# Optimization experiments

Hardware: AMD Instinct MI355X
Metric: run time of the kernel (lower is better)

Reference implementation:

```python
import jax, jax.numpy as jnp
import numpy as np

EMBED_DIM = 256
NUM_HEADS = 8
HEAD_DIM = EMBED_DIM // NUM_HEADS
ADJ_CHANNELS = 4
B, N = 8, 1024


def setup_inputs() -> dict:
    key = jax.random.key(0)
    ks = jax.random.split(key, 12)
    s = 1.0 / np.sqrt(EMBED_DIM)
    sa = 1.0 / np.sqrt(ADJ_CHANNELS)
    return {
        "x": jax.random.normal(ks[0], (B, N, EMBED_DIM), dtype=jnp.float32),
        "adj": jax.random.uniform(ks[1], (B, N, N, ADJ_CHANNELS), dtype=jnp.float32),
        "Wq": jax.random.uniform(ks[2], (EMBED_DIM, EMBED_DIM), jnp.float32, -s, s),
        "bq": jnp.zeros((EMBED_DIM,), jnp.float32),
        "Wk": jax.random.uniform(ks[3], (EMBED_DIM, EMBED_DIM), jnp.float32, -s, s),
        "bk": jnp.zeros((EMBED_DIM,), jnp.float32),
        "Wv": jax.random.uniform(ks[4], (EMBED_DIM, EMBED_DIM), jnp.float32, -s, s),
        "bv": jnp.zeros((EMBED_DIM,), jnp.float32),
        "Wo": jax.random.uniform(ks[5], (EMBED_DIM, EMBED_DIM), jnp.float32, -s, s),
        "bo": jnp.zeros((EMBED_DIM,), jnp.float32),
        "Wa": jax.random.uniform(ks[6], (ADJ_CHANNELS, NUM_HEADS), jnp.float32, -sa, sa),
        "ba": jnp.zeros((NUM_HEADS,), jnp.float32),
    }


def reference(x, adj, Wq, bq, Wk, bk, Wv, bv, Wo, bo, Wa, ba):
    Bs, Ns, E = x.shape
    H, D = NUM_HEADS, HEAD_DIM
    def heads(W, b):
        return (x @ W + b).reshape(Bs, Ns, H, D).transpose(0, 2, 1, 3)  # [B,H,N,D]
    Q, K, V = heads(Wq, bq), heads(Wk, bk), heads(Wv, bv)
    # adjacency-derived additive bias: [B,N,N,C] -> [B,N,N,H] -> [B,H,N,N]
    bias = jnp.moveaxis(adj @ Wa + ba, -1, 1)
    scores = jnp.einsum("bhnd,bhmd->bhnm", Q, K) / np.sqrt(D) + bias
    attn = jax.nn.softmax(scores, axis=-1)
    ctx = jnp.einsum("bhnm,bhmd->bhnd", attn, V)  # [B,H,N,D]
    ctx = ctx.transpose(0, 2, 1, 3).reshape(Bs, Ns, E)
    return ctx @ Wo + bo + x
```

## Files before the change

### kernel.cpp

```cpp
#include <hip/hip_runtime.h>
#include <hip/hip_bf16.h>

#define BATCH 8
#define SEQ   1024
#define EMB   256
#define NH    8
#define HD    32
#define QSCALE 0.2550030053f

typedef __attribute__((ext_vector_type(8))) short short8;
typedef __attribute__((ext_vector_type(4))) float floatx4;

__device__ __forceinline__ ushort f2bf(float f) {
    __hip_bfloat16 h = __float2bfloat16(f);
    return *reinterpret_cast<ushort*>(&h);
}

__device__ __forceinline__ void gload_lds16(const float4* g, float4* l) {
    __builtin_amdgcn_global_load_lds(
        (const __attribute__((address_space(1))) unsigned int*)g,
        (__attribute__((address_space(3))) unsigned int*)l, 16, 0, 0);
}

__global__ __launch_bounds__(256) void prep_kernel(
    const float* __restrict__ Wq, const float* __restrict__ Wk,
    const float* __restrict__ Wv, const float* __restrict__ Wo,
    ushort* __restrict__ Wqt, ushort* __restrict__ Wkt,
    ushort* __restrict__ Wvt, ushort* __restrict__ Wot)
{
    __shared__ float tilebuf[32][33];
    const int blk = blockIdx.x;
    const int mat = blk >> 6, tile = blk & 63;
    const int ti = tile >> 3, tj = tile & 7;
    const float* W = (mat == 0) ? Wq : (mat == 1) ? Wk : (mat == 2) ? Wv : Wo;
    ushort* Wt = (mat == 0) ? Wqt : (mat == 1) ? Wkt : (mat == 2) ? Wvt : Wot;
    const float scale = (mat == 0) ? QSCALE : 1.0f;

    const int tx = threadIdx.x & 31, ty = threadIdx.x >> 5;
    #pragma unroll
    for (int p = 0; p < 4; ++p)
        tilebuf[ty + p * 8][tx] = W[(size_t)(ti * 32 + ty + p * 8) * EMB + tj * 32 + tx];
    __syncthreads();
    #pragma unroll
    for (int p = 0; p < 4; ++p)
        Wt[(size_t)(tj * 32 + ty + p * 8) * EMB + ti * 32 + tx] =
            f2bf(tilebuf[tx][ty + p * 8] * scale);
}

__global__ __launch_bounds__(256) void qkv_gemm(
    const float* __restrict__ x,
    const ushort* __restrict__ Wqt, const ushort* __restrict__ Wkt,
    const ushort* __restrict__ Wvt,
    const float* __restrict__ bq, const float* __restrict__ bk,
    const float* __restrict__ bv,
    ushort* __restrict__ Qb, ushort* __restrict__ Kb, ushort* __restrict__ Vt)
{
    const int mat = blockIdx.y;
    const ushort* __restrict__ Wt = (mat == 0) ? Wqt : (mat == 1) ? Wkt : Wvt;
    const float* __restrict__ bias = (mat == 0) ? bq : (mat == 1) ? bk : bv;
    const float bscale = (mat == 0) ? QSCALE : 1.0f;

    const int w = threadIdx.x >> 6, lane = threadIdx.x & 63;
    const int quad = lane >> 4, l16 = lane & 15;
    const int row0 = blockIdx.x * 64 + w * 16;

    floatx4 acc[16];
    #pragma unroll
    for (int i = 0; i < 16; ++i) acc[i] = (floatx4){0.f, 0.f, 0.f, 0.f};

    const float* __restrict__ xrow = x + (size_t)(row0 + l16) * EMB + quad * 8;

    #pragma unroll
    for (int ks = 0; ks < 8; ++ks) {
        const float4 xa0 = *(const float4*)(xrow + ks * 32);
        const float4 xa1 = *(const float4*)(xrow + ks * 32 + 4);
        ushort au[8] = {f2bf(xa0.x), f2bf(xa0.y), f2bf(xa0.z), f2bf(xa0.w),
                        f2bf(xa1.x), f2bf(xa1.y), f2bf(xa1.z), f2bf(xa1.w)};
        const short8 a = *(const short8*)au;
        #pragma unroll
        for (int i = 0; i < 16; ++i) {
            const short8 bf = *(const short8*)(Wt + (size_t)(i * 16 + l16) * EMB + ks * 32 + quad * 8);
            acc[i] = __builtin_amdgcn_mfma_f32_16x16x32_bf16(a, bf, acc[i], 0, 0, 0);
        }
    }

    const int gr0 = row0 + quad * 4;
    if (mat < 2) {
        ushort* __restrict__ dst = (mat == 0) ? Qb : Kb;
        #pragma unroll
        for (int i = 0; i < 16; ++i) {
            const int c = i * 16 + l16, h = c >> 5, d = c & (HD - 1);
            const float bb = bias[c] * bscale;
            #pragma unroll
            for (int r = 0; r < 4; ++r) {
                const int gr = gr0 + r, b = gr >> 10, n = gr & (SEQ - 1);
                dst[((size_t)(b * NH + h) * SEQ + n) * HD + d] = f2bf(acc[i][r] + bb);
            }
        }
    } else {
        const int b = gr0 >> 10, n0 = gr0 & (SEQ - 1);
        const int j0 = n0 & 31;
        const int slot = (j0 < 16) ? ((j0 >> 2) << 3)
                                   : ((((j0 - 16) >> 2) << 3) + 4);
        const int nperm = (n0 & ~31) | slot;
        #pragma unroll
        for (int i = 0; i < 16; ++i) {
            const int c = i * 16 + l16, h = c >> 5, d = c & (HD - 1);
            const float bb = bias[c];
            ushort4 t4;
            t4.x = f2bf(acc[i][0] + bb); t4.y = f2bf(acc[i][1] + bb);
            t4.z = f2bf(acc[i][2] + bb); t4.w = f2bf(acc[i][3] + bb);
            *(ushort4*)(Vt + ((size_t)(b * NH + h) * HD + d) * SEQ + nperm) = t4;
        }
    }
}

__global__ __launch_bounds__(512) void attn_kernel(
    const ushort* __restrict__ Qb, const ushort* __restrict__ Kb,
    const ushort* __restrict__ Vt, const float* __restrict__ adj,
    const float* __restrict__ Wa, const float* __restrict__ ba,
    float* __restrict__ cp, float* __restrict__ lsum)
{
    __shared__ float4 Atile[2][16][65];
    const int tid = threadIdx.x, h = tid >> 6, lane = tid & 63;
    const int quad = lane >> 4, l16 = lane & 15;
    const int q0 = blockIdx.x * 16, b = blockIdx.y, z = blockIdx.z;
    const int bh = b * NH + h;
    const int kz = z * 512;

    const float LOG2E = 1.4426950408889634f;
    const float wa0 = Wa[0 * NH + h] * LOG2E, wa1 = Wa[1 * NH + h] * LOG2E;
    const float wa2 = Wa[2 * NH + h] * LOG2E, wa3 = Wa[3 * NH + h] * LOG2E;
    const float bah = ba[h] * LOG2E;

    const short8 aq = *(const short8*)(Qb + ((size_t)bh * SEQ + q0 + l16) * HD + quad * 8);

    floatx4 o0 = {0.f, 0.f, 0.f, 0.f}, o1 = {0.f, 0.f, 0.f, 0.f};
    float lacc = 0.f;

    const float4* __restrict__ adjb = (const float4*)adj + (size_t)b * SEQ * SEQ;
    const float4* __restrict__ asrc0 = adjb + (size_t)(q0 + 2 * h)     * SEQ + kz + lane;
    const float4* __restrict__ asrc1 = adjb + (size_t)(q0 + 2 * h + 1) * SEQ + kz + lane;

    const ushort* __restrict__ Kbase = Kb + (size_t)bh * SEQ * HD + (size_t)l16 * HD + quad * 8;
    const ushort* __restrict__ Vb0 = Vt + ((size_t)bh * HD + l16) * SEQ + quad * 8;
    const ushort* __restrict__ Vb1 = Vt + ((size_t)bh * HD + 16 + l16) * SEQ + quad * 8;

    gload_lds16(asrc0, &Atile[0][2 * h][0]);
    gload_lds16(asrc1, &Atile[0][2 * h + 1][0]);
    __syncthreads();

    for (int it = 0; it < 8; ++it) {
        const int cur = it & 1;
        const int key0 = kz + it * 64;

        if (it < 7) {
            gload_lds16(asrc0 + (it + 1) * 64, &Atile[cur ^ 1][2 * h][0]);
            gload_lds16(asrc1 + (it + 1) * 64, &Atile[cur ^ 1][2 * h + 1][0]);
        }

        const short8 k0 = *(const short8*)(Kbase + (size_t)(key0)      * HD);
        const short8 k1 = *(const short8*)(Kbase + (size_t)(key0 + 16) * HD);
        const short8 k2 = *(const short8*)(Kbase + (size_t)(key0 + 32) * HD);
        const short8 k3 = *(const short8*)(Kbase + (size_t)(key0 + 48) * HD);
        const floatx4 zz = {0.f, 0.f, 0.f, 0.f};
        floatx4 s0 = __builtin_amdgcn_mfma_f32_16x16x32_bf16(k0, aq, zz, 0, 0, 0);
        floatx4 s1 = __builtin_amdgcn_mfma_f32_16x16x32_bf16(k1, aq, zz, 0, 0, 0);
        floatx4 s2 = __builtin_amdgcn_mfma_f32_16x16x32_bf16(k2, aq, zz, 0, 0, 0);
        floatx4 s3 = __builtin_amdgcn_mfma_f32_16x16x32_bf16(k3, aq, zz, 0, 0, 0);

        ushort pu0[8], pu1[8];
        #pragma unroll
        for (int r = 0; r < 4; ++r) {
            const int col = 4 * quad + r;
            const float4 a0 = Atile[cur][l16][col];
            const float4 a1 = Atile[cur][l16][16 + col];
            const float4 a2 = Atile[cur][l16][32 + col];
            const float4 a3 = Atile[cur][l16][48 + col];
            const float b0 = fmaf(a0.x, wa0, fmaf(a0.y, wa1, fmaf(a0.z, wa2, fmaf(a0.w, wa3, bah))));
            const float b1 = fmaf(a1.x, wa0, fmaf(a1.y, wa1, fmaf(a1.z, wa2, fmaf(a1.w, wa3, bah))));
            const float b2 = fmaf(a2.x, wa0, fmaf(a2.y, wa1, fmaf(a2.z, wa2, fmaf(a2.w, wa3, bah))));
            const float b3 = fmaf(a3.x, wa0, fmaf(a3.y, wa1, fmaf(a3.z, wa2, fmaf(a3.w, wa3, bah))));
            const float p0 = exp2f(s0[r] + b0);
            const float p1 = exp2f(s1[r] + b1);
            const float p2 = exp2f(s2[r] + b2);
            const float p3 = exp2f(s3[r] + b3);
            lacc += (p0 + p1) + (p2 + p3);
            pu0[r]     = f2bf(p0);
            pu0[4 + r] = f2bf(p1);
            pu1[r]     = f2bf(p2);
            pu1[4 + r] = f2bf(p3);
        }
        const short8 pf0 = *(const short8*)pu0;
        const short8 pf1 = *(const short8*)pu1;

        const short8 v00 = *(const short8*)(Vb0 + key0);
        const short8 v10 = *(const short8*)(Vb1 + key0);
        const short8 v01 = *(const short8*)(Vb0 + key0 + 32);
        const short8 v11 = *(const short8*)(Vb1 + key0 + 32);
        o0 = __builtin_amdgcn_mfma_f32_16x16x32_bf16(v00, pf0, o0, 0, 0, 0);
        o1 = __builtin_amdgcn_mfma_f32_16x16x32_bf16(v10, pf0, o1, 0, 0, 0);
        o0 = __builtin_amdgcn_mfma_f32_16x16x32_bf16(v01, pf1, o0, 0, 0, 0);
        o1 = __builtin_amdgcn_mfma_f32_16x16x32_bf16(v11, pf1, o1, 0, 0, 0);

        __syncthreads();
    }

    lacc += __shfl_xor(lacc, 16, 64);
    lacc += __shfl_xor(lacc, 32, 64);

    float* __restrict__ cpz = cp + (size_t)z * BATCH * SEQ * EMB;
    float* __restrict__ lsz = lsum + (size_t)z * BATCH * SEQ * NH;
    const size_t grow = (size_t)b * SEQ + q0 + l16;
    *(floatx4*)(cpz + grow * EMB + h * HD + 4 * quad)      = o0;
    *(floatx4*)(cpz + grow * EMB + h * HD + 16 + 4 * quad) = o1;
    if (quad == 0) lsz[grow * NH + h] = lacc;
}

__global__ __launch_bounds__(256) void outproj_gemm(
    const float* __restrict__ cp, const float* __restrict__ lsum,
    const ushort* __restrict__ Wot, const float* __restrict__ bo,
    const float* __restrict__ x, float* __restrict__ out)
{
    const int w = threadIdx.x >> 6, lane = threadIdx.x & 63;
    const int quad = lane >> 4, l16 = lane & 15;
    const int row0 = blockIdx.x * 64 + w * 16;
    const int c0 = blockIdx.y * 128;
    const int arow = row0 + l16;
    const float* __restrict__ cp1 = cp + (size_t)BATCH * SEQ * EMB;
    const float* __restrict__ l1  = lsum + (size_t)BATCH * SEQ * NH;

    floatx4 acc[8];
    #pragma unroll
    for (int i = 0; i < 8; ++i) acc[i] = (floatx4){0.f, 0.f, 0.f, 0.f};

    #pragma unroll
    for (int ks = 0; ks < 8; ++ks) {
        const float invl = 1.0f / (lsum[(size_t)arow * NH + ks] + l1[(size_t)arow * NH + ks]);
        const size_t cb = (size_t)arow * EMB + ks * 32 + quad * 8;
        const float4 c00 = *(const float4*)(cp + cb);
        const float4 c01 = *(const float4*)(cp + cb + 4);
        const float4 c10 = *(const float4*)(cp1 + cb);
        const float4 c11 = *(const float4*)(cp1 + cb + 4);
        ushort au[8] = {
            f2bf((c00.x + c10.x) * invl), f2bf((c00.y + c10.y) * invl),
            f2bf((c00.z + c10.z) * invl), f2bf((c00.w + c10.w) * invl),
            f2bf((c01.x + c11.x) * invl), f2bf((c01.y + c11.y) * invl),
            f2bf((c01.z + c11.z) * invl), f2bf((c01.w + c11.w) * invl)};
        const short8 a = *(const short8*)au;
        #pragma unroll
        for (int i = 0; i < 8; ++i) {
            const short8 bfr = *(const short8*)(Wot + (size_t)(c0 + i * 16 + l16) * EMB + ks * 32 + quad * 8);
            acc[i] = __builtin_amdgcn_mfma_f32_16x16x32_bf16(a, bfr, acc[i], 0, 0, 0);
        }
    }

    const int gr0 = row0 + quad * 4;
    #pragma unroll
    for (int i = 0; i < 8; ++i) {
        const int c = c0 + i * 16 + l16;
        const float bov = bo[c];
        #pragma unroll
        for (int r = 0; r < 4; ++r) {
            const size_t idx = (size_t)(gr0 + r) * EMB + c;
            out[idx] = acc[i][r] + bov + x[idx];
        }
    }
}

extern "C" void kernel_launch(void* const* d_in, const int* in_sizes, int n_in,
                              void* d_out, int out_size, void* d_ws, size_t ws_size,
                              hipStream_t stream) {
    const float* x   = (const float*)d_in[0];
    const float* adj = (const float*)d_in[1];
    const float* Wq  = (const float*)d_in[2];
    const float* bq  = (const float*)d_in[3];
    const float* Wk  = (const float*)d_in[4];
    const float* bk  = (const float*)d_in[5];
    const float* Wv  = (const float*)d_in[6];
    const float* bv  = (const float*)d_in[7];
    const float* Wo  = (const float*)d_in[8];
    const float* bo  = (const float*)d_in[9];
    const float* Wa  = (const float*)d_in[10];
    const float* ba  = (const float*)d_in[11];

    const size_t per = (size_t)BATCH * NH * SEQ * HD;
    ushort* Qb  = (ushort*)d_ws;
    ushort* Kb  = Qb + per;
    ushort* Vt  = Kb + per;
    ushort* Wqt = Vt + per;
    ushort* Wkt = Wqt + EMB * EMB;
    ushort* Wvt = Wkt + EMB * EMB;
    ushort* Wot = Wvt + EMB * EMB;
    float*  cp  = (float*)(Wot + EMB * EMB);
    float*  ls  = cp + 2 * (size_t)BATCH * SEQ * EMB;

    prep_kernel<<<256, 256, 0, stream>>>(Wq, Wk, Wv, Wo, Wqt, Wkt, Wvt, Wot);
    qkv_gemm<<<dim3(BATCH * SEQ / 64, 3), 256, 0, stream>>>(
        x, Wqt, Wkt, Wvt, bq, bk, bv, Qb, Kb, Vt);
    attn_kernel<<<dim3(SEQ / 16, BATCH, 2), 512, 0, stream>>>(
        Qb, Kb, Vt, adj, Wa, ba, cp, ls);
    outproj_gemm<<<dim3(BATCH * SEQ / 64, 2), 256, 0, stream>>>(
        cp, ls, Wot, bo, x, (float*)d_out);
}
```

Before: 287.9 us.

## Load adjacency directly from global per head, dropping LDS staging and barriers

```diff
diff --git a/kernel.cpp b/kernel.cpp
--- a/kernel.cpp
+++ b/kernel.cpp
@@ -14,12 +14,6 @@
 __device__ __forceinline__ ushort f2bf(float f) {
     __hip_bfloat16 h = __float2bfloat16(f);
     return *reinterpret_cast<ushort*>(&h);
-}
-
-__device__ __forceinline__ void gload_lds16(const float4* g, float4* l) {
-    __builtin_amdgcn_global_load_lds(
-        (const __attribute__((address_space(1))) unsigned int*)g,
-        (__attribute__((address_space(3))) unsigned int*)l, 16, 0, 0);
 }
 
 __global__ __launch_bounds__(256) void prep_kernel(
@@ -121,7 +115,6 @@
     const float* __restrict__ Wa, const float* __restrict__ ba,
     float* __restrict__ cp, float* __restrict__ lsum)
 {
-    __shared__ float4 Atile[2][16][65];
     const int tid = threadIdx.x, h = tid >> 6, lane = tid & 63;
     const int quad = lane >> 4, l16 = lane & 15;
     const int q0 = blockIdx.x * 16, b = blockIdx.y, z = blockIdx.z;
@@ -138,26 +131,17 @@
     floatx4 o0 = {0.f, 0.f, 0.f, 0.f}, o1 = {0.f, 0.f, 0.f, 0.f};
     float lacc = 0.f;
 
-    const float4* __restrict__ adjb = (const float4*)adj + (size_t)b * SEQ * SEQ;
-    const float4* __restrict__ asrc0 = adjb + (size_t)(q0 + 2 * h)     * SEQ + kz + lane;
-    const float4* __restrict__ asrc1 = adjb + (size_t)(q0 + 2 * h + 1) * SEQ + kz + lane;
+    const float4* __restrict__ arow = (const float4*)adj + (size_t)b * SEQ * SEQ
+                                    + (size_t)(q0 + l16) * SEQ + kz + 4 * quad;
 
     const ushort* __restrict__ Kbase = Kb + (size_t)bh * SEQ * HD + (size_t)l16 * HD + quad * 8;
     const ushort* __restrict__ Vb0 = Vt + ((size_t)bh * HD + l16) * SEQ + quad * 8;
     const ushort* __restrict__ Vb1 = Vt + ((size_t)bh * HD + 16 + l16) * SEQ + quad * 8;
 
-    gload_lds16(asrc0, &Atile[0][2 * h][0]);
-    gload_lds16(asrc1, &Atile[0][2 * h + 1][0]);
-    __syncthreads();
-
+    #pragma unroll 2
     for (int it = 0; it < 8; ++it) {
-        const int cur = it & 1;
         const int key0 = kz + it * 64;
-
-        if (it < 7) {
-            gload_lds16(asrc0 + (it + 1) * 64, &Atile[cur ^ 1][2 * h][0]);
-            gload_lds16(asrc1 + (it + 1) * 64, &Atile[cur ^ 1][2 * h + 1][0]);
-        }
+        const int c0 = it * 64;
 
         const short8 k0 = *(const short8*)(Kbase + (size_t)(key0)      * HD);
         const short8 k1 = *(const short8*)(Kbase + (size_t)(key0 + 16) * HD);
@@ -172,11 +156,10 @@
         ushort pu0[8], pu1[8];
         #pragma unroll
         for (int r = 0; r < 4; ++r) {
-            const int col = 4 * quad + r;
-            const float4 a0 = Atile[cur][l16][col];
-            const float4 a1 = Atile[cur][l16][16 + col];
-            const float4 a2 = Atile[cur][l16][32 + col];
-            const float4 a3 = Atile[cur][l16][48 + col];
+            const float4 a0 = arow[c0 + r];
+            const float4 a1 = arow[c0 + 16 + r];
+            const float4 a2 = arow[c0 + 32 + r];
+            const float4 a3 = arow[c0 + 48 + r];
             const float b0 = fmaf(a0.x, wa0, fmaf(a0.y, wa1, fmaf(a0.z, wa2, fmaf(a0.w, wa3, bah))));
             const float b1 = fmaf(a1.x, wa0, fmaf(a1.y, wa1, fmaf(a1.z, wa2, fmaf(a1.w, wa3, bah))));
             const float b2 = fmaf(a2.x, wa0, fmaf(a2.y, wa1, fmaf(a2.z, wa2, fmaf(a2.w, wa3, bah))));
@@ -202,8 +185,6 @@
         o1 = __builtin_amdgcn_mfma_f32_16x16x32_bf16(v10, pf0, o1, 0, 0, 0);
         o0 = __builtin_amdgcn_mfma_f32_16x16x32_bf16(v01, pf1, o0, 0, 0, 0);
         o1 = __builtin_amdgcn_mfma_f32_16x16x32_bf16(v11, pf1, o1, 0, 0, 0);
-
-        __syncthreads();
     }
 
     lacc += __shfl_xor(lacc, 16, 64);
```

Measured after the change: 395.7 us. 1.37x slower.
